# Kernel optimization log

Hardware: AMD Instinct MI355X
Metric: run time of the kernel (lower is better)

The kernel has to match this reference:

```python
import jax, jax.numpy as jnp
import numpy as np

N, E, D, EDIM = 50000, 800000, 128, 1
LN_EPS = 1e-5
NORM_FACTOR = 1.0


def _ln(x, g, b):
    m = jnp.mean(x, axis=-1, keepdims=True)
    v = jnp.var(x, axis=-1, keepdims=True)
    return (x - m) * jax.lax.rsqrt(v + LN_EPS) * g + b


def _mlp(x, w1, b1, g, be, w2, b2):
    # Linear -> SiLU -> LayerNorm -> Linear (matches nn.Sequential in msg_net/out_net)
    h = jax.nn.silu(x @ w1 + b1)
    h = _ln(h, g, be)
    return h @ w2 + b2


def setup_inputs() -> dict:
    key = jax.random.key(0)
    ks = jax.random.split(key, 24)
    s = 1.0 / np.sqrt(D)
    sa = 1.0 / np.sqrt(2 * D + EDIM)
    f32 = jnp.float32
    return {
        "h": jax.random.normal(ks[0], (N, D), f32),
        "edge_attr": jax.random.uniform(ks[1], (E, EDIM), f32),
        "row": jax.random.randint(ks[2], (E,), 0, N),
        "col": jax.random.randint(ks[3], (E,), 0, N),
        "node_mask": jnp.ones((N, 1), f32),
        "edge_mask": jnp.ones((E, 1), f32),
        "lin_w": jax.random.normal(ks[4], (D, D), f32) * s,
        "lin_b": jnp.zeros((D,), f32),
        "msg_w1": jax.random.normal(ks[5], (D, D), f32) * s,
        "msg_b1": jnp.zeros((D,), f32),
        "msg_ln_g": jnp.ones((D,), f32),
        "msg_ln_b": jnp.zeros((D,), f32),
        "msg_w2": jax.random.normal(ks[6], (D, D), f32) * s,
        "msg_b2": jnp.zeros((D,), f32),
        "att_w1": jax.random.normal(ks[7], (2 * D + EDIM, D), f32) * sa,
        "att_b1": jnp.zeros((D,), f32),
        "att_w2": jax.random.normal(ks[8], (D, 1), f32) * s,
        "att_b2": jnp.zeros((1,), f32),
        "out_w1": jax.random.normal(ks[9], (D, D), f32) * s,
        "out_b1": jnp.zeros((D,), f32),
        "out_ln_g": jnp.ones((D,), f32),
        "out_ln_b": jnp.zeros((D,), f32),
        "out_w2": jax.random.normal(ks[10], (D, D), f32) * s,
        "out_b2": jnp.zeros((D,), f32),
        "ln_g": jnp.ones((D,), f32),
        "ln_b": jnp.zeros((D,), f32),
    }


def reference(h, edge_attr, row, col, node_mask, edge_mask,
              lin_w, lin_b,
              msg_w1, msg_b1, msg_ln_g, msg_ln_b, msg_w2, msg_b2,
              att_w1, att_b1, att_w2, att_b2,
              out_w1, out_b1, out_ln_g, out_ln_b, out_w2, out_b2,
              ln_g, ln_b):
    # h = self.linear(h)
    x = h @ lin_w + lin_b                                    # [N, D]
    # msg_net transform of node features
    x_ = _mlp(x, msg_w1, msg_b1, msg_ln_g, msg_ln_b, msg_w2, msg_b2)
    # DenseAtt: cat(x[row], x[col], edge_attr) -> MLP -> sigmoid -> * edge_mask
    feat = jnp.concatenate([x[row], x[col], edge_attr], axis=1)   # [E, 2D+edge_dim]
    att = jax.nn.sigmoid(jax.nn.silu(feat @ att_w1 + att_b1) @ att_w2 + att_b2)
    att = att * edge_mask                                    # [E, 1]
    # gather -> weighted message -> scatter_add (unsorted_segment_sum, 'sum' norm)
    msg = jax.ops.segment_sum(x_[col] * att, row, num_segments=N) / NORM_FACTOR
    # out_net transform, residual, final LayerNorm
    msg = _mlp(msg, out_w1, out_b1, out_ln_g, out_ln_b, out_w2, out_b2)
    return _ln(x + msg, ln_g, ln_b)                          # [N, D]
```

## Files before the change

kernel.cpp:

```cpp
#include <hip/hip_runtime.h>

#define LN_EPS 1e-5f

typedef __attribute__((ext_vector_type(8))) short short8;
typedef __attribute__((ext_vector_type(4))) float f32x4;

__device__ __forceinline__ float sigf(float x) {
    return __builtin_amdgcn_rcpf(1.0f + __expf(-x));
}

__device__ __forceinline__ unsigned short f2bf(float f) {
    unsigned u = __float_as_uint(f);
    return (unsigned short)((u + 0x7fffu + ((u >> 16) & 1u)) >> 16);
}
__device__ __forceinline__ unsigned f2bf2(float lo, float hi) {
    return (unsigned)f2bf(lo) | ((unsigned)f2bf(hi) << 16);
}
__device__ __forceinline__ void bf2f(unsigned u, float& lo, float& hi) {
    lo = __uint_as_float(u << 16);
    hi = __uint_as_float(u & 0xffff0000u);
}
__device__ __forceinline__ void bf8f(uint4 p, float* o) {
    bf2f(p.x, o[0], o[1]); bf2f(p.y, o[2], o[3]);
    bf2f(p.z, o[4], o[5]); bf2f(p.w, o[6], o[7]);
}
__device__ __forceinline__ float bf1f(unsigned short s) {
    return __uint_as_float(((unsigned)s) << 16);
}

__device__ __forceinline__ float quad_add_all(float x) {
    int v = __builtin_amdgcn_update_dpp(0, __float_as_int(x), 0xB1, 0xF, 0xF, true);
    x += __int_as_float(v);
    v = __builtin_amdgcn_update_dpp(0, __float_as_int(x), 0x4E, 0xF, 0xF, true);
    x += __int_as_float(v);
    return x;
}

__global__ __launch_bounds__(256)
void prep_w(const float* __restrict__ lin_w, const float* __restrict__ msg_w1,
            const float* __restrict__ msg_w2, const float* __restrict__ att_w1,
            const float* __restrict__ out_w1, const float* __restrict__ out_w2,
            const float* __restrict__ att_b1, unsigned short* __restrict__ wp,
            float* __restrict__ bias256)
{
    const int idx = blockIdx.x * 256 + threadIdx.x;
    if (idx < 8 * 16384) {
        const int m = idx >> 14, r = idx & 16383;
        const int k = r >> 7, n = r & 127;
        const float* src; int slot; int fnBase = 0;
        switch (m) {
            case 0: src = lin_w;  slot = 0; break;
            case 1: src = msg_w1; slot = 1; break;
            case 2: src = msg_w2; slot = 2; break;
            case 3: src = att_w1; slot = 3; break;
            case 4: src = att_w1 + 128 * 128; slot = 3; fnBase = 8; break;
            case 5: src = out_w1; slot = 5; break;
            default: src = out_w2; slot = 6; break;
        }
        const float v = src[k * 128 + n];
        const int fn = fnBase + (n >> 4);
        const int fk = k >> 5, kb = (k >> 3) & 3, j = k & 7;
        const size_t dst = (size_t)slot * 16384 + ((size_t)((fn * 4 + fk) * 64 + (n & 15) + 16 * kb)) * 8 + j;
        wp[dst] = f2bf(v);
    } else if (idx < 8 * 16384 + 256) {
        const int t = idx - 8 * 16384;
        bias256[t] = (t < 128) ? att_b1[t] : 0.f;
    }
}

__device__ __forceinline__ short8 ldA_bf(const unsigned short* A, size_t row, int k0) {
    return *(const short8*)(A + row * 128 + k0);
}
__device__ __forceinline__ short8 ldA_f32(const float* A, size_t row, int k0) {
    const float* ap = A + row * 128 + k0;
    const float4 f0 = *(const float4*)ap;
    const float4 f1 = *(const float4*)(ap + 4);
    union { unsigned u[4]; short8 s; } v;
    v.u[0] = f2bf2(f0.x, f0.y); v.u[1] = f2bf2(f0.z, f0.w);
    v.u[2] = f2bf2(f1.x, f1.y); v.u[3] = f2bf2(f1.z, f1.w);
    return v.s;
}

template<int NFN, int ABF, int SPLIT>
__global__ __launch_bounds__(256, NFN == 8 ? 4 : 3)
void gemm_mfma(const void* __restrict__ Av, const unsigned short* __restrict__ Wp,
               const float* __restrict__ bias,
               unsigned short* __restrict__ C1, int ld1,
               unsigned short* __restrict__ C2, int ld2, int nrows)
{
    const int tid = threadIdx.x;
    const int w = tid >> 6, lane = tid & 63;
    const int r0 = blockIdx.x * 64;
    const int arow = r0 + w * 16 + (lane & 15);
    const size_t rowc = (arow < nrows) ? (size_t)arow : (size_t)(nrows - 1);
    const int kh = (lane >> 4) * 8;

    short8 a[4];
#pragma unroll
    for (int fk = 0; fk < 4; ++fk)
        a[fk] = ABF ? ldA_bf((const unsigned short*)Av, rowc, fk * 32 + kh)
                    : ldA_f32((const float*)Av, rowc, fk * 32 + kh);

    const short8* Bf = (const short8*)Wp;
    f32x4 acc[NFN];
#pragma unroll
    for (int fn = 0; fn < NFN; ++fn) acc[fn] = (f32x4){0.f, 0.f, 0.f, 0.f};
#pragma unroll
    for (int fk = 0; fk < 4; ++fk)
#pragma unroll
        for (int fn = 0; fn < NFN; ++fn)
            acc[fn] = __builtin_amdgcn_mfma_f32_16x16x32_bf16(a[fk], Bf[(fn * 4 + fk) * 64 + lane], acc[fn], 0, 0, 0);

    const int cn = lane & 15, rq = lane >> 4;
    float bv[NFN];
#pragma unroll
    for (int fn = 0; fn < NFN; ++fn) bv[fn] = bias ? bias[fn * 16 + cn] : 0.f;

#pragma unroll
    for (int reg = 0; reg < 4; ++reg) {
        const int gr = r0 + w * 16 + rq * 4 + reg;
        if (gr < nrows) {
#pragma unroll
            for (int fn = 0; fn < NFN; ++fn) {
                const float v = acc[fn][reg] + bv[fn];
                if (SPLIT) {
                    if (fn < 8) C1[(size_t)gr * ld1 + fn * 16 + cn] = f2bf(v);
                    else        C2[(size_t)gr * ld2 + (fn - 8) * 16 + cn] = f2bf(v);
                } else {
                    C1[(size_t)gr * ld1 + fn * 16 + cn] = f2bf(v);
                }
            }
        }
    }
}

template<int EPI2>
__global__ __launch_bounds__(256, 4)
void gemm2_mfma(const unsigned short* __restrict__ Av,
                const unsigned short* __restrict__ Wp1, const float* __restrict__ b1,
                const float* __restrict__ ln1g, const float* __restrict__ ln1b,
                const unsigned short* __restrict__ Wp2, const float* __restrict__ b2,
                const float* __restrict__ ln2g, const float* __restrict__ ln2b,
                const unsigned short* __restrict__ resH, void* __restrict__ Cv, int nrows)
{
    __shared__ unsigned short hof[4 * 2048];
    const int tid = threadIdx.x;
    const int w = tid >> 6, lane = tid & 63;
    const int r0 = blockIdx.x * 64;
    const int arow = r0 + w * 16 + (lane & 15);
    const size_t rowc = (arow < nrows) ? (size_t)arow : (size_t)(nrows - 1);
    const int kh = (lane >> 4) * 8;
    const int cn = lane & 15, rq = lane >> 4;

    short8 a[4];
#pragma unroll
    for (int fk = 0; fk < 4; ++fk)
        a[fk] = ldA_bf(Av, rowc, fk * 32 + kh);

    const short8* B1f = (const short8*)Wp1;
    f32x4 acc[8];
#pragma unroll
    for (int fn = 0; fn < 8; ++fn) acc[fn] = (f32x4){0.f, 0.f, 0.f, 0.f};
#pragma unroll
    for (int fk = 0; fk < 4; ++fk)
#pragma unroll
        for (int fn = 0; fn < 8; ++fn)
            acc[fn] = __builtin_amdgcn_mfma_f32_16x16x32_bf16(a[fk], B1f[(fn * 4 + fk) * 64 + lane], acc[fn], 0, 0, 0);

    unsigned short* hw = hof + w * 2048;
    {
        float bv[8], gv[8], bbv[8];
#pragma unroll
        for (int fn = 0; fn < 8; ++fn) {
            bv[fn] = b1[fn * 16 + cn]; gv[fn] = ln1g[fn * 16 + cn]; bbv[fn] = ln1b[fn * 16 + cn];
        }
#pragma unroll
        for (int reg = 0; reg < 4; ++reg) {
            float val[8];
            float sum = 0.f, sq = 0.f;
#pragma unroll
            for (int fn = 0; fn < 8; ++fn) {
                float v = acc[fn][reg] + bv[fn];
                v = v * sigf(v);
                val[fn] = v; sum += v; sq += v * v;
            }
#pragma unroll
            for (int m = 1; m < 16; m <<= 1) { sum += __shfl_xor(sum, m); sq += __shfl_xor(sq, m); }
            const float mean = sum * (1.f / 128.f);
            const float var = sq * (1.f / 128.f) - mean * mean;
            const float rstd = rsqrtf(var + LN_EPS);
            const int row16 = rq * 4 + reg;
            const int sw = (row16 & 7) << 3;
#pragma unroll
            for (int fn = 0; fn < 8; ++fn) {
                const float o = (val[fn] - mean) * rstd * gv[fn] + bbv[fn];
                hw[row16 * 128 + ((fn * 16 + cn) ^ sw)] = f2bf(o);
            }
        }
    }

    short8 a2[4];
    {
        const int row16 = lane & 15;
        const int sw = (row16 & 7) << 3;
#pragma unroll
        for (int fk = 0; fk < 4; ++fk)
            a2[fk] = *(const short8*)(hw + row16 * 128 + ((fk * 32 + kh) ^ sw));
    }

    const short8* B2f = (const short8*)Wp2;
    f32x4 acc2[8];
#pragma unroll
    for (int fn = 0; fn < 8; ++fn) acc2[fn] = (f32x4){0.f, 0.f, 0.f, 0.f};
#pragma unroll
    for (int fk = 0; fk < 4; ++fk)
#pragma unroll
        for (int fn = 0; fn < 8; ++fn)
            acc2[fn] = __builtin_amdgcn_mfma_f32_16x16x32_bf16(a2[fk], B2f[(fn * 4 + fk) * 64 + lane], acc2[fn], 0, 0, 0);

    float bv2[8];
#pragma unroll
    for (int fn = 0; fn < 8; ++fn) bv2[fn] = b2[fn * 16 + cn];

    if (EPI2 == 0) {
        unsigned short* Ch = (unsigned short*)Cv;
#pragma unroll
        for (int reg = 0; reg < 4; ++reg) {
            const int gr = r0 + w * 16 + rq * 4 + reg;
            if (gr < nrows) {
#pragma unroll
                for (int fn = 0; fn < 8; ++fn)
                    Ch[(size_t)gr * 128 + fn * 16 + cn] = f2bf(acc2[fn][reg] + bv2[fn]);
            }
        }
    } else {
        float* Cf = (float*)Cv;
        float gv[8], bbv[8];
#pragma unroll
        for (int fn = 0; fn < 8; ++fn) { gv[fn] = ln2g[fn * 16 + cn]; bbv[fn] = ln2b[fn * 16 + cn]; }
#pragma unroll
        for (int reg = 0; reg < 4; ++reg) {
            const int gr = r0 + w * 16 + rq * 4 + reg;
            const int grc = gr < nrows ? gr : nrows - 1;
            float val[8];
            float sum = 0.f, sq = 0.f;
#pragma unroll
            for (int fn = 0; fn < 8; ++fn) {
                float v = acc2[fn][reg] + bv2[fn] + bf1f(resH[(size_t)grc * 128 + fn * 16 + cn]);
                val[fn] = v; sum += v; sq += v * v;
            }
#pragma unroll
            for (int m = 1; m < 16; m <<= 1) { sum += __shfl_xor(sum, m); sq += __shfl_xor(sq, m); }
            const float mean = sum * (1.f / 128.f);
            const float var = sq * (1.f / 128.f) - mean * mean;
            const float rstd = rsqrtf(var + LN_EPS);
            if (gr < nrows) {
#pragma unroll
                for (int fn = 0; fn < 8; ++fn)
                    Cf[(size_t)gr * 128 + fn * 16 + cn] = (val[fn] - mean) * rstd * gv[fn] + bbv[fn];
            }
        }
    }
}

__global__ __launch_bounds__(256)
void hist_rank(const int* __restrict__ row, int* __restrict__ cnt,
               int* __restrict__ rank, int E)
{
    const int tid = blockIdx.x * blockDim.x + threadIdx.x;
    const int stride = gridDim.x * blockDim.x;
    for (int e0 = tid; e0 < E; e0 += stride * 4) {
        int r[4]; bool val[4];
#pragma unroll
        for (int u = 0; u < 4; ++u) {
            const int e = e0 + u * stride;
            val[u] = e < E;
            r[u] = val[u] ? row[e] : 0;
        }
        int rk[4];
#pragma unroll
        for (int u = 0; u < 4; ++u)
            if (val[u]) rk[u] = atomicAdd(&cnt[r[u]], 1);
#pragma unroll
        for (int u = 0; u < 4; ++u)
            if (val[u]) rank[e0 + u * stride] = rk[u];
    }
}

__global__ __launch_bounds__(1024)
void scan_a(const int* __restrict__ cnt, int* __restrict__ off,
            int* __restrict__ btot, int n)
{
    __shared__ int wsum[16];
    const int tid = threadIdx.x, lane = tid & 63, wv = tid >> 6;
    const int i = blockIdx.x * 1024 + tid;
    const int v = (i < n) ? cnt[i] : 0;
    int incl = v;
#pragma unroll
    for (int d = 1; d < 64; d <<= 1) { int t = __shfl_up(incl, d); if (lane >= d) incl += t; }
    if (lane == 63) wsum[wv] = incl;
    __syncthreads();
    if (tid == 0) {
        int run = 0;
        for (int ww = 0; ww < 16; ++ww) { int t = wsum[ww]; wsum[ww] = run; run += t; }
    }
    __syncthreads();
    if (i < n) off[i] = wsum[wv] + incl - v;
    if (tid == 1023) btot[blockIdx.x] = wsum[15] + incl;
}

__global__ __launch_bounds__(64)
void scan_b(int* __restrict__ btot, int* __restrict__ bexc,
            int* __restrict__ off, int n, int nb, int E)
{
    const int t = threadIdx.x;
    const int v = (t < nb) ? btot[t] : 0;
    int incl = v;
#pragma unroll
    for (int d = 1; d < 64; d <<= 1) { int u = __shfl_up(incl, d); if (t >= d) incl += u; }
    if (t < nb) bexc[t] = incl - v;
    if (t == 0) off[n] = E;
}

__global__ __launch_bounds__(1024)
void scan_c(int* __restrict__ off, const int* __restrict__ bexc, int n)
{
    const int i = blockIdx.x * 1024 + threadIdx.x;
    if (i < n) off[i] += bexc[blockIdx.x];
}

__global__ __launch_bounds__(256, 4)
void att_edge(const unsigned short* __restrict__ xrH,
              const unsigned short* __restrict__ xcH,
              const int* __restrict__ row, const int* __restrict__ col,
              const float* __restrict__ ea, const float* __restrict__ em,
              const int* __restrict__ rank, const int* __restrict__ off,
              const float* __restrict__ we_, const float* __restrict__ w2_,
              const float* __restrict__ b2p, uint2* __restrict__ catS, int E)
{
    const int lane = threadIdx.x & 63;
    const int q = lane & 3;
    const int gwid = (blockIdx.x * blockDim.x + threadIdx.x) >> 6;
    const int nw = (gridDim.x * blockDim.x) >> 6;

    float we[32], w2[32];
#pragma unroll
    for (int ch = 0; ch < 4; ++ch) {
        const float4 a0 = ((const float4*)we_)[ch * 8 + q * 2];
        const float4 a1 = ((const float4*)we_)[ch * 8 + q * 2 + 1];
        we[ch * 8 + 0] = a0.x; we[ch * 8 + 1] = a0.y; we[ch * 8 + 2] = a0.z; we[ch * 8 + 3] = a0.w;
        we[ch * 8 + 4] = a1.x; we[ch * 8 + 5] = a1.y; we[ch * 8 + 6] = a1.z; we[ch * 8 + 7] = a1.w;
        const float4 c0 = ((const float4*)w2_)[ch * 8 + q * 2];
        const float4 c1 = ((const float4*)w2_)[ch * 8 + q * 2 + 1];
        w2[ch * 8 + 0] = c0.x; w2[ch * 8 + 1] = c0.y; w2[ch * 8 + 2] = c0.z; w2[ch * 8 + 3] = c0.w;
        w2[ch * 8 + 4] = c1.x; w2[ch * 8 + 5] = c1.y; w2[ch * 8 + 6] = c1.z; w2[ch * 8 + 7] = c1.w;
    }
    const float b2 = *b2p;

    for (int base = gwid * 16; base < E; base += nw * 16) {
        const int e = base + (lane >> 2);
        const bool valid = e < E;
        const int ec = valid ? e : E - 1;
        const int r = row[ec], c = col[ec];
        const float eax = ea[ec], emv = em[ec];
        const unsigned short* xr = xrH + (size_t)r * 128;
        const unsigned short* xc = xcH + (size_t)c * 128;
        float p = 0.f;
#pragma unroll
        for (int ch = 0; ch < 4; ++ch) {
            const uint4 pa = *(const uint4*)(xr + ch * 32 + q * 8);
            const uint4 pb = *(const uint4*)(xc + ch * 32 + q * 8);
            float xa[8], xb[8];
            bf8f(pa, xa); bf8f(pb, xb);
#pragma unroll
            for (int i = 0; i < 8; ++i) {
                const float t = xa[i] + xb[i] + eax * we[ch * 8 + i];
                p += t * sigf(t) * w2[ch * 8 + i];
            }
        }
        p = quad_add_all(p);
        const float att = sigf(p + b2) * emv;
        if (valid && q == 0) {
            const int pos = off[r] + rank[ec];
            catS[pos] = make_uint2((unsigned)c, __float_as_uint(att));
        }
    }
}

__global__ __launch_bounds__(256)
void accum_k(const unsigned short* __restrict__ xmH, const int* __restrict__ off,
             const uint2* __restrict__ catS, unsigned short* __restrict__ msgH, int N)
{
    const int lane = threadIdx.x & 63;
    const int g = lane >> 4, l = lane & 15;
    const int gwid = (blockIdx.x * blockDim.x + threadIdx.x) >> 6;
    const int nw = (gridDim.x * blockDim.x) >> 6;
    const uint4* xm4 = (const uint4*)xmH;

    for (int wid = gwid; wid < N; wid += nw) {
        int j0 = off[wid];
        const int jend = off[wid + 1];
        float acc[8] = {0.f, 0.f, 0.f, 0.f, 0.f, 0.f, 0.f, 0.f};

        for (; j0 + 16 <= jend; j0 += 16) {
            uint2 ca[4]; uint4 pk[4];
#pragma unroll
            for (int u = 0; u < 4; ++u) ca[u] = catS[j0 + u * 4 + g];
#pragma unroll
            for (int u = 0; u < 4; ++u) pk[u] = xm4[(size_t)ca[u].x * 16 + l];
#pragma unroll
            for (int u = 0; u < 4; ++u) {
                const float att = __uint_as_float(ca[u].y);
                float xm[8];
                bf8f(pk[u], xm);
#pragma unroll
                for (int i = 0; i < 8; ++i) acc[i] = fmaf(att, xm[i], acc[i]);
            }
        }
        for (; j0 + 8 <= jend; j0 += 8) {
            const uint2 caA = catS[j0 + g];
            const uint2 caB = catS[j0 + 4 + g];
            const uint4 pA = xm4[(size_t)caA.x * 16 + l];
            const uint4 pB = xm4[(size_t)caB.x * 16 + l];
            const float attA = __uint_as_float(caA.y);
            const float attB = __uint_as_float(caB.y);
            float xmA[8], xmB[8];
            bf8f(pA, xmA); bf8f(pB, xmB);
#pragma unroll
            for (int i = 0; i < 8; ++i)
                acc[i] = fmaf(attB, xmB[i], fmaf(attA, xmA[i], acc[i]));
        }
        for (; j0 < jend; j0 += 4) {
            const int je = j0 + g;
            const bool valid = je < jend;
            const int jc = valid ? je : jend - 1;
            const uint2 ca = catS[jc];
            const uint4 p = xm4[(size_t)ca.x * 16 + l];
            const float att = valid ? __uint_as_float(ca.y) : 0.f;
            float xm[8];
            bf8f(p, xm);
#pragma unroll
            for (int i = 0; i < 8; ++i) acc[i] = fmaf(att, xm[i], acc[i]);
        }

#pragma unroll
        for (int i = 0; i < 8; ++i) {
            acc[i] += __shfl_xor(acc[i], 16);
            acc[i] += __shfl_xor(acc[i], 32);
        }
        if (g == 0) {
            uint4 pk;
            pk.x = f2bf2(acc[0], acc[1]); pk.y = f2bf2(acc[2], acc[3]);
            pk.z = f2bf2(acc[4], acc[5]); pk.w = f2bf2(acc[6], acc[7]);
            ((uint4*)msgH)[(size_t)wid * 16 + l] = pk;
        }
    }
}

extern "C" void kernel_launch(void* const* d_in, const int* in_sizes, int n_in,
                              void* d_out, int out_size, void* d_ws, size_t ws_size,
                              hipStream_t stream)
{
    const float* h        = (const float*)d_in[0];
    const float* edge_attr= (const float*)d_in[1];
    const int*   row      = (const int*)d_in[2];
    const int*   col      = (const int*)d_in[3];
    const float* edge_mask= (const float*)d_in[5];
    const float* lin_w    = (const float*)d_in[6];
    const float* lin_b    = (const float*)d_in[7];
    const float* msg_w1   = (const float*)d_in[8];
    const float* msg_b1   = (const float*)d_in[9];
    const float* msg_ln_g = (const float*)d_in[10];
    const float* msg_ln_b = (const float*)d_in[11];
    const float* msg_w2   = (const float*)d_in[12];
    const float* msg_b2   = (const float*)d_in[13];
    const float* att_w1   = (const float*)d_in[14];
    const float* att_b1   = (const float*)d_in[15];
    const float* att_w2   = (const float*)d_in[16];
    const float* att_b2   = (const float*)d_in[17];
    const float* out_w1   = (const float*)d_in[18];
    const float* out_b1   = (const float*)d_in[19];
    const float* out_ln_g = (const float*)d_in[20];
    const float* out_ln_b = (const float*)d_in[21];
    const float* out_w2   = (const float*)d_in[22];
    const float* out_b2   = (const float*)d_in[23];
    const float* ln_g     = (const float*)d_in[24];
    const float* ln_b     = (const float*)d_in[25];

    const int N = in_sizes[0] / 128;
    const int E = in_sizes[2];
    const size_t NF = (size_t)N * 128;

    unsigned short* xbH  = (unsigned short*)d_ws;
    unsigned short* xrH  = xbH + NF;
    unsigned short* xcH  = xrH + NF;
    unsigned short* xmH  = xcH + NF;
    unsigned short* msgH = xmH + NF;
    int*    cnt   = (int*)(msgH + NF);
    int*    off   = cnt + N;
    int*    btot  = off + N + 8;
    int*    bexc  = btot + 64;
    int*    rank  = bexc + 64;
    uint2*  catS  = (uint2*)(rank + E);
    unsigned short* wp = (unsigned short*)(catS + E);
    float* bias256 = (float*)(wp + 8 * 16384);

    const int gb = (N + 63) / 64;
    const int nb = (N + 1023) / 1024;
    const int hgrid = (E + 256 * 4 - 1) / (256 * 4);

    prep_w<<<513, 256, 0, stream>>>(lin_w, msg_w1, msg_w2, att_w1, out_w1, out_w2,
                                    att_b1, wp, bias256);
    hipMemsetAsync(cnt, 0, (size_t)N * sizeof(int), stream);
    hist_rank<<<hgrid, 256, 0, stream>>>(row, cnt, rank, E);
    scan_a<<<nb, 1024, 0, stream>>>(cnt, off, btot, N);
    scan_b<<<1, 64, 0, stream>>>(btot, bexc, off, N, nb, E);
    scan_c<<<nb, 1024, 0, stream>>>(off, bexc, N);

    gemm_mfma<8, 0, 0><<<gb, 256, 0, stream>>>(h, wp, lin_b, xbH, 128, nullptr, 0, N);
    gemm_mfma<16, 1, 1><<<gb, 256, 0, stream>>>(xbH, wp + 3 * 16384, bias256, xrH, 128, xcH, 128, N);
    att_edge<<<2048, 256, 0, stream>>>(xrH, xcH, row, col, edge_attr, edge_mask,
                                       rank, off, att_w1 + 256 * 128, att_w2, att_b2,
                                       catS, E);

    gemm2_mfma<0><<<gb, 256, 0, stream>>>(xbH, wp + 16384, msg_b1, msg_ln_g, msg_ln_b,
                                          wp + 2 * 16384, msg_b2, nullptr, nullptr,
                                          nullptr, xmH, N);

    accum_k<<<2048, 256, 0, stream>>>(xmH, off, catS, msgH, N);

    gemm2_mfma<3><<<gb, 256, 0, stream>>>(msgH, wp + 5 * 16384, out_b1, out_ln_g, out_ln_b,
                                          wp + 6 * 16384, out_b2, ln_g, ln_b,
                                          xbH, (float*)d_out, N);
}
```

Measured before the change: 231.5 us.

## Fuse node-side linear, attention projection and message MLP into one kernel

Merges the three node-level GEMM kernels (input linear, attention row/col projections, msg MLP) into a single front kernel. The linear output stays in LDS and is reused as the MFMA A-operand instead of being re-read from global memory, which also removes two launches. The hist_rank unroll goes from 4 to 8 and the attention dot-product is split into per-chunk partial sums. The fused kernel holds more accumulators and two LDS buffers, so register pressure could limit occupancy.

```diff
diff --git a/kernel.cpp b/kernel.cpp
--- a/kernel.cpp
+++ b/kernel.cpp
@@ -68,9 +68,6 @@
     }
 }
 
-__device__ __forceinline__ short8 ldA_bf(const unsigned short* A, size_t row, int k0) {
-    return *(const short8*)(A + row * 128 + k0);
-}
 __device__ __forceinline__ short8 ldA_f32(const float* A, size_t row, int k0) {
     const float* ap = A + row * 128 + k0;
     const float4 f0 = *(const float4*)ap;
@@ -80,68 +77,184 @@
     v.u[2] = f2bf2(f1.x, f1.y); v.u[3] = f2bf2(f1.z, f1.w);
     return v.s;
 }
-
-template<int NFN, int ABF, int SPLIT>
-__global__ __launch_bounds__(256, NFN == 8 ? 4 : 3)
-void gemm_mfma(const void* __restrict__ Av, const unsigned short* __restrict__ Wp,
-               const float* __restrict__ bias,
-               unsigned short* __restrict__ C1, int ld1,
-               unsigned short* __restrict__ C2, int ld2, int nrows)
-{
+__device__ __forceinline__ short8 ldA_bf(const unsigned short* A, size_t row, int k0) {
+    return *(const short8*)(A + row * 128 + k0);
+}
+
+__global__ __launch_bounds__(256, 4)
+void front_mfma(const float* __restrict__ h,
+                const unsigned short* __restrict__ WpLin, const float* __restrict__ lin_b,
+                const unsigned short* __restrict__ WpAtt, const float* __restrict__ bias256,
+                const unsigned short* __restrict__ WpM1, const float* __restrict__ msg_b1,
+                const float* __restrict__ m1g, const float* __restrict__ m1b,
+                const unsigned short* __restrict__ WpM2, const float* __restrict__ msg_b2,
+                unsigned short* __restrict__ xbH, unsigned short* __restrict__ xrH,
+                unsigned short* __restrict__ xcH, unsigned short* __restrict__ xmH,
+                int nrows)
+{
+    __shared__ unsigned short hofA[4 * 2048];
+    __shared__ unsigned short hofB[4 * 2048];
     const int tid = threadIdx.x;
     const int w = tid >> 6, lane = tid & 63;
     const int r0 = blockIdx.x * 64;
     const int arow = r0 + w * 16 + (lane & 15);
     const size_t rowc = (arow < nrows) ? (size_t)arow : (size_t)(nrows - 1);
     const int kh = (lane >> 4) * 8;
+    const int cn = lane & 15, rq = lane >> 4;
+    unsigned short* hwA = hofA + w * 2048;
+    unsigned short* hwB = hofB + w * 2048;
 
     short8 a[4];
 #pragma unroll
-    for (int fk = 0; fk < 4; ++fk)
-        a[fk] = ABF ? ldA_bf((const unsigned short*)Av, rowc, fk * 32 + kh)
-                    : ldA_f32((const float*)Av, rowc, fk * 32 + kh);
-
-    const short8* Bf = (const short8*)Wp;
-    f32x4 acc[NFN];
-#pragma unroll
-    for (int fn = 0; fn < NFN; ++fn) acc[fn] = (f32x4){0.f, 0.f, 0.f, 0.f};
-#pragma unroll
-    for (int fk = 0; fk < 4; ++fk)
-#pragma unroll
-        for (int fn = 0; fn < NFN; ++fn)
-            acc[fn] = __builtin_amdgcn_mfma_f32_16x16x32_bf16(a[fk], Bf[(fn * 4 + fk) * 64 + lane], acc[fn], 0, 0, 0);
-
-    const int cn = lane & 15, rq = lane >> 4;
-    float bv[NFN];
-#pragma unroll
-    for (int fn = 0; fn < NFN; ++fn) bv[fn] = bias ? bias[fn * 16 + cn] : 0.f;
-
-#pragma unroll
-    for (int reg = 0; reg < 4; ++reg) {
-        const int gr = r0 + w * 16 + rq * 4 + reg;
-        if (gr < nrows) {
-#pragma unroll
-            for (int fn = 0; fn < NFN; ++fn) {
-                const float v = acc[fn][reg] + bv[fn];
-                if (SPLIT) {
-                    if (fn < 8) C1[(size_t)gr * ld1 + fn * 16 + cn] = f2bf(v);
-                    else        C2[(size_t)gr * ld2 + (fn - 8) * 16 + cn] = f2bf(v);
-                } else {
-                    C1[(size_t)gr * ld1 + fn * 16 + cn] = f2bf(v);
+    for (int fk = 0; fk < 4; ++fk) a[fk] = ldA_f32(h, rowc, fk * 32 + kh);
+
+    {
+        const short8* Bf = (const short8*)WpLin;
+        f32x4 accx[8];
+#pragma unroll
+        for (int fn = 0; fn < 8; ++fn) accx[fn] = (f32x4){0.f, 0.f, 0.f, 0.f};
+#pragma unroll
+        for (int fk = 0; fk < 4; ++fk)
+#pragma unroll
+            for (int fn = 0; fn < 8; ++fn)
+                accx[fn] = __builtin_amdgcn_mfma_f32_16x16x32_bf16(a[fk], Bf[(fn * 4 + fk) * 64 + lane], accx[fn], 0, 0, 0);
+
+        float bv[8];
+#pragma unroll
+        for (int fn = 0; fn < 8; ++fn) bv[fn] = lin_b[fn * 16 + cn];
+#pragma unroll
+        for (int reg = 0; reg < 4; ++reg) {
+            const int gr = r0 + w * 16 + rq * 4 + reg;
+            const int row16 = rq * 4 + reg;
+            const int sw = (row16 & 7) << 3;
+#pragma unroll
+            for (int fn = 0; fn < 8; ++fn) {
+                const unsigned short hb = f2bf(accx[fn][reg] + bv[fn]);
+                if (gr < nrows) xbH[(size_t)gr * 128 + fn * 16 + cn] = hb;
+                hwA[row16 * 128 + ((fn * 16 + cn) ^ sw)] = hb;
+            }
+        }
+    }
+
+    short8 ax[4];
+    {
+        const int row16 = lane & 15;
+        const int sw = (row16 & 7) << 3;
+#pragma unroll
+        for (int fk = 0; fk < 4; ++fk)
+            ax[fk] = *(const short8*)(hwA + row16 * 128 + ((fk * 32 + kh) ^ sw));
+    }
+
+    {
+        const short8* Bf = (const short8*)WpAtt;
+        f32x4 acca[16];
+#pragma unroll
+        for (int fn = 0; fn < 16; ++fn) acca[fn] = (f32x4){0.f, 0.f, 0.f, 0.f};
+#pragma unroll
+        for (int fk = 0; fk < 4; ++fk)
+#pragma unroll
+            for (int fn = 0; fn < 16; ++fn)
+                acca[fn] = __builtin_amdgcn_mfma_f32_16x16x32_bf16(ax[fk], Bf[(fn * 4 + fk) * 64 + lane], acca[fn], 0, 0, 0);
+
+        float bv[16];
+#pragma unroll
+        for (int fn = 0; fn < 16; ++fn) bv[fn] = bias256[fn * 16 + cn];
+#pragma unroll
+        for (int reg = 0; reg < 4; ++reg) {
+            const int gr = r0 + w * 16 + rq * 4 + reg;
+            if (gr < nrows) {
+#pragma unroll
+                for (int fn = 0; fn < 16; ++fn) {
+                    const float v = acca[fn][reg] + bv[fn];
+                    if (fn < 8) xrH[(size_t)gr * 128 + fn * 16 + cn] = f2bf(v);
+                    else        xcH[(size_t)gr * 128 + (fn - 8) * 16 + cn] = f2bf(v);
                 }
             }
         }
     }
-}
-
-template<int EPI2>
+
+    {
+        const short8* Bf = (const short8*)WpM1;
+        f32x4 acc1[8];
+#pragma unroll
+        for (int fn = 0; fn < 8; ++fn) acc1[fn] = (f32x4){0.f, 0.f, 0.f, 0.f};
+#pragma unroll
+        for (int fk = 0; fk < 4; ++fk)
+#pragma unroll
+            for (int fn = 0; fn < 8; ++fn)
+                acc1[fn] = __builtin_amdgcn_mfma_f32_16x16x32_bf16(ax[fk], Bf[(fn * 4 + fk) * 64 + lane], acc1[fn], 0, 0, 0);
+
+        float bv[8], gv[8], bbv[8];
+#pragma unroll
+        for (int fn = 0; fn < 8; ++fn) {
+            bv[fn] = msg_b1[fn * 16 + cn]; gv[fn] = m1g[fn * 16 + cn]; bbv[fn] = m1b[fn * 16 + cn];
+        }
+#pragma unroll
+        for (int reg = 0; reg < 4; ++reg) {
+            float val[8];
+            float sum = 0.f, sq = 0.f;
+#pragma unroll
+            for (int fn = 0; fn < 8; ++fn) {
+                float v = acc1[fn][reg] + bv[fn];
+                v = v * sigf(v);
+                val[fn] = v; sum += v; sq += v * v;
+            }
+#pragma unroll
+            for (int m = 1; m < 16; m <<= 1) { sum += __shfl_xor(sum, m); sq += __shfl_xor(sq, m); }
+            const float mean = sum * (1.f / 128.f);
+            const float var = sq * (1.f / 128.f) - mean * mean;
+            const float rstd = rsqrtf(var + LN_EPS);
+            const int row16 = rq * 4 + reg;
+            const int sw = (row16 & 7) << 3;
+#pragma unroll
+            for (int fn = 0; fn < 8; ++fn) {
+                const float o = (val[fn] - mean) * rstd * gv[fn] + bbv[fn];
+                hwB[row16 * 128 + ((fn * 16 + cn) ^ sw)] = f2bf(o);
+            }
+        }
+    }
+
+    short8 am[4];
+    {
+        const int row16 = lane & 15;
+        const int sw = (row16 & 7) << 3;
+#pragma unroll
+        for (int fk = 0; fk < 4; ++fk)
+            am[fk] = *(const short8*)(hwB + row16 * 128 + ((fk * 32 + kh) ^ sw));
+    }
+    {
+        const short8* Bf = (const short8*)WpM2;
+        f32x4 acc2[8];
+#pragma unroll
+        for (int fn = 0; fn < 8; ++fn) acc2[fn] = (f32x4){0.f, 0.f, 0.f, 0.f};
+#pragma unroll
+        for (int fk = 0; fk < 4; ++fk)
+#pragma unroll
+            for (int fn = 0; fn < 8; ++fn)
+                acc2[fn] = __builtin_amdgcn_mfma_f32_16x16x32_bf16(am[fk], Bf[(fn * 4 + fk) * 64 + lane], acc2[fn], 0, 0, 0);
+
+        float bv[8];
+#pragma unroll
+        for (int fn = 0; fn < 8; ++fn) bv[fn] = msg_b2[fn * 16 + cn];
+#pragma unroll
+        for (int reg = 0; reg < 4; ++reg) {
+            const int gr = r0 + w * 16 + rq * 4 + reg;
+            if (gr < nrows) {
+#pragma unroll
+                for (int fn = 0; fn < 8; ++fn)
+                    xmH[(size_t)gr * 128 + fn * 16 + cn] = f2bf(acc2[fn][reg] + bv[fn]);
+            }
+        }
+    }
+}
+
 __global__ __launch_bounds__(256, 4)
 void gemm2_mfma(const unsigned short* __restrict__ Av,
                 const unsigned short* __restrict__ Wp1, const float* __restrict__ b1,
                 const float* __restrict__ ln1g, const float* __restrict__ ln1b,
                 const unsigned short* __restrict__ Wp2, const float* __restrict__ b2,
                 const float* __restrict__ ln2g, const float* __restrict__ ln2b,
-                const unsigned short* __restrict__ resH, void* __restrict__ Cv, int nrows)
+                const unsigned short* __restrict__ resH, float* __restrict__ Cf, int nrows)
 {
     __shared__ unsigned short hof[4 * 2048];
     const int tid = threadIdx.x;
@@ -154,8 +267,7 @@
 
     short8 a[4];
 #pragma unroll
-    for (int fk = 0; fk < 4; ++fk)
-        a[fk] = ldA_bf(Av, rowc, fk * 32 + kh);
+    for (int fk = 0; fk < 4; ++fk) a[fk] = ldA_bf(Av, rowc, fk * 32 + kh);
 
     const short8* B1f = (const short8*)Wp1;
     f32x4 acc[8];
@@ -218,47 +330,31 @@
         for (int fn = 0; fn < 8; ++fn)
             acc2[fn] = __builtin_amdgcn_mfma_f32_16x16x32_bf16(a2[fk], B2f[(fn * 4 + fk) * 64 + lane], acc2[fn], 0, 0, 0);
 
-    float bv2[8];
-#pragma unroll
-    for (int fn = 0; fn < 8; ++fn) bv2[fn] = b2[fn * 16 + cn];
-
-    if (EPI2 == 0) {
-        unsigned short* Ch = (unsigned short*)Cv;
-#pragma unroll
-        for (int reg = 0; reg < 4; ++reg) {
-            const int gr = r0 + w * 16 + rq * 4 + reg;
-            if (gr < nrows) {
-#pragma unroll
-                for (int fn = 0; fn < 8; ++fn)
-                    Ch[(size_t)gr * 128 + fn * 16 + cn] = f2bf(acc2[fn][reg] + bv2[fn]);
-            }
-        }
-    } else {
-        float* Cf = (float*)Cv;
-        float gv[8], bbv[8];
-#pragma unroll
-        for (int fn = 0; fn < 8; ++fn) { gv[fn] = ln2g[fn * 16 + cn]; bbv[fn] = ln2b[fn * 16 + cn]; }
-#pragma unroll
-        for (int reg = 0; reg < 4; ++reg) {
-            const int gr = r0 + w * 16 + rq * 4 + reg;
-            const int grc = gr < nrows ? gr : nrows - 1;
-            float val[8];
-            float sum = 0.f, sq = 0.f;
-#pragma unroll
-            for (int fn = 0; fn < 8; ++fn) {
-                float v = acc2[fn][reg] + bv2[fn] + bf1f(resH[(size_t)grc * 128 + fn * 16 + cn]);
-                val[fn] = v; sum += v; sq += v * v;
-            }
-#pragma unroll
-            for (int m = 1; m < 16; m <<= 1) { sum += __shfl_xor(sum, m); sq += __shfl_xor(sq, m); }
-            const float mean = sum * (1.f / 128.f);
-            const float var = sq * (1.f / 128.f) - mean * mean;
-            const float rstd = rsqrtf(var + LN_EPS);
-            if (gr < nrows) {
-#pragma unroll
-                for (int fn = 0; fn < 8; ++fn)
-                    Cf[(size_t)gr * 128 + fn * 16 + cn] = (val[fn] - mean) * rstd * gv[fn] + bbv[fn];
-            }
+    float bv2[8], gv[8], bbv[8];
+#pragma unroll
+    for (int fn = 0; fn < 8; ++fn) {
+        bv2[fn] = b2[fn * 16 + cn]; gv[fn] = ln2g[fn * 16 + cn]; bbv[fn] = ln2b[fn * 16 + cn];
+    }
+#pragma unroll
+    for (int reg = 0; reg < 4; ++reg) {
+        const int gr = r0 + w * 16 + rq * 4 + reg;
+        const int grc = gr < nrows ? gr : nrows - 1;
+        float val[8];
+        float sum = 0.f, sq = 0.f;
+#pragma unroll
+        for (int fn = 0; fn < 8; ++fn) {
+            float v = acc2[fn][reg] + bv2[fn] + bf1f(resH[(size_t)grc * 128 + fn * 16 + cn]);
+            val[fn] = v; sum += v; sq += v * v;
+        }
+#pragma unroll
+        for (int m = 1; m < 16; m <<= 1) { sum += __shfl_xor(sum, m); sq += __shfl_xor(sq, m); }
+        const float mean = sum * (1.f / 128.f);
+        const float var = sq * (1.f / 128.f) - mean * mean;
+        const float rstd = rsqrtf(var + LN_EPS);
+        if (gr < nrows) {
+#pragma unroll
+            for (int fn = 0; fn < 8; ++fn)
+                Cf[(size_t)gr * 128 + fn * 16 + cn] = (val[fn] - mean) * rstd * gv[fn] + bbv[fn];
         }
     }
 }
@@ -269,20 +365,20 @@
 {
     const int tid = blockIdx.x * blockDim.x + threadIdx.x;
     const int stride = gridDim.x * blockDim.x;
-    for (int e0 = tid; e0 < E; e0 += stride * 4) {
-        int r[4]; bool val[4];
-#pragma unroll
-        for (int u = 0; u < 4; ++u) {
+    for (int e0 = tid; e0 < E; e0 += stride * 8) {
+        int r[8]; bool val[8];
+#pragma unroll
+        for (int u = 0; u < 8; ++u) {
             const int e = e0 + u * stride;
             val[u] = e < E;
             r[u] = val[u] ? row[e] : 0;
         }
-        int rk[4];
-#pragma unroll
-        for (int u = 0; u < 4; ++u)
+        int rk[8];
+#pragma unroll
+        for (int u = 0; u < 8; ++u)
             if (val[u]) rk[u] = atomicAdd(&cnt[r[u]], 1);
 #pragma unroll
-        for (int u = 0; u < 4; ++u)
+        for (int u = 0; u < 8; ++u)
             if (val[u]) rank[e0 + u * stride] = rk[u];
     }
 }
@@ -365,19 +461,22 @@
         const float eax = ea[ec], emv = em[ec];
         const unsigned short* xr = xrH + (size_t)r * 128;
         const unsigned short* xc = xcH + (size_t)c * 128;
-        float p = 0.f;
+        float pc[4];
 #pragma unroll
         for (int ch = 0; ch < 4; ++ch) {
             const uint4 pa = *(const uint4*)(xr + ch * 32 + q * 8);
             const uint4 pb = *(const uint4*)(xc + ch * 32 + q * 8);
             float xa[8], xb[8];
             bf8f(pa, xa); bf8f(pb, xb);
+            float s = 0.f;
 #pragma unroll
             for (int i = 0; i < 8; ++i) {
                 const float t = xa[i] + xb[i] + eax * we[ch * 8 + i];
-                p += t * sigf(t) * w2[ch * 8 + i];
-            }
-        }
+                s += t * sigf(t) * w2[ch * 8 + i];
+            }
+            pc[ch] = s;
+        }
+        float p = (pc[0] + pc[1]) + (pc[2] + pc[3]);
         p = quad_add_all(p);
         const float att = sigf(p + b2) * emv;
         if (valid && q == 0) {
@@ -507,7 +606,7 @@
 
     const int gb = (N + 63) / 64;
     const int nb = (N + 1023) / 1024;
-    const int hgrid = (E + 256 * 4 - 1) / (256 * 4);
+    const int hgrid = (E + 256 * 8 - 1) / (256 * 8);
 
     prep_w<<<513, 256, 0, stream>>>(lin_w, msg_w1, msg_w2, att_w1, out_w1, out_w2,
                                     att_b1, wp, bias256);
@@ -517,19 +616,19 @@
     scan_b<<<1, 64, 0, stream>>>(btot, bexc, off, N, nb, E);
     scan_c<<<nb, 1024, 0, stream>>>(off, bexc, N);
 
-    gemm_mfma<8, 0, 0><<<gb, 256, 0, stream>>>(h, wp, lin_b, xbH, 128, nullptr, 0, N);
-    gemm_mfma<16, 1, 1><<<gb, 256, 0, stream>>>(xbH, wp + 3 * 16384, bias256, xrH, 128, xcH, 128, N);
+    front_mfma<<<gb, 256, 0, stream>>>(h, wp, lin_b,
+                                       wp + 3 * 16384, bias256,
+                                       wp + 16384, msg_b1, msg_ln_g, msg_ln_b,
+                                       wp + 2 * 16384, msg_b2,
+                                       xbH, xrH, xcH, xmH, N);
+
     att_edge<<<2048, 256, 0, stream>>>(xrH, xcH, row, col, edge_attr, edge_mask,
                                        rank, off, att_w1 + 256 * 128, att_w2, att_b2,
                                        catS, E);
 
-    gemm2_mfma<0><<<gb, 256, 0, stream>>>(xbH, wp + 16384, msg_b1, msg_ln_g, msg_ln_b,
-                                          wp + 2 * 16384, msg_b2, nullptr, nullptr,
-                                          nullptr, xmH, N);
-
     accum_k<<<2048, 256, 0, stream>>>(xmH, off, catS, msgH, N);
 
-    gemm2_mfma<3><<<gb, 256, 0, stream>>>(msgH, wp + 5 * 16384, out_b1, out_ln_g, out_ln_b,
-                                          wp + 6 * 16384, out_b2, ln_g, ln_b,
-                                          xbH, (float*)d_out, N);
-}
+    gemm2_mfma<<<gb, 256, 0, stream>>>(msgH, wp + 5 * 16384, out_b1, out_ln_g, out_ln_b,
+                                       wp + 6 * 16384, out_b2, ln_g, ln_b,
+                                       xbH, (float*)d_out, N);
+}
```

New measurement: 230.9 us. Within noise of the previous version (-0.3%).
